# Kernel optimization log

Measured on AMD Instinct MI355X. Metric: run time of the kernel, lower is better.

Reference implementation:

```python
import jax, jax.numpy as jnp
import numpy as np

N_NODES = 100000
N_EDGES = 1600000
N_ETYPES = 3
IN_FEATS = 128
HEADS = 4
OUT_FEATS = 16
EDGE_FEATS = 64
NEG_SLOPE = 0.2


def setup_inputs() -> dict:
    key = jax.random.key(0)
    ks = jax.random.split(key, 10)
    return {
        "x": jax.random.normal(ks[0], (N_NODES, IN_FEATS), jnp.float32),
        "W": jax.random.normal(ks[1], (IN_FEATS, HEADS * OUT_FEATS), jnp.float32) * 0.05,
        "W_e": jax.random.normal(ks[2], (EDGE_FEATS, HEADS * EDGE_FEATS), jnp.float32) * 0.05,
        "attn_l": jax.random.normal(ks[3], (HEADS, OUT_FEATS), jnp.float32) * 0.1,
        "attn_r": jax.random.normal(ks[4], (HEADS, OUT_FEATS), jnp.float32) * 0.1,
        "attn_e": jax.random.normal(ks[5], (HEADS, EDGE_FEATS), jnp.float32) * 0.1,
        "edge_emb": jax.random.normal(ks[6], (N_ETYPES, EDGE_FEATS), jnp.float32),
        "src": jax.random.randint(ks[7], (N_EDGES,), 0, N_NODES, jnp.int32),
        "dst": jax.random.randint(ks[8], (N_EDGES,), 0, N_NODES, jnp.int32),
        "etype": jax.random.randint(ks[9], (N_EDGES,), 0, N_ETYPES, jnp.int32),
    }


def reference(x, W, W_e, attn_l, attn_r, attn_e, edge_emb, src, dst, etype):
    N = x.shape[0]
    H, D = attn_l.shape
    # node projection: [N, H, D]
    feat = (x @ W).reshape(N, H, D)
    # per-node attention halves: [N, H]
    el = jnp.einsum("nhd,hd->nh", feat, attn_l)
    er = jnp.einsum("nhd,hd->nh", feat, attn_r)
    # per-etype edge term: [T, H]
    e_feat = (edge_emb @ W_e).reshape(edge_emb.shape[0], H, -1)
    ee = jnp.einsum("the,he->th", e_feat, attn_e)
    # per-edge pre-softmax score: [E, H]
    s = el[src] + er[dst] + ee[etype]
    s = jnp.where(s > 0, s, NEG_SLOPE * s)  # leaky_relu
    # edge softmax over incoming edges of each dst node (homogeneous graph)
    m = jax.ops.segment_max(s, dst, num_segments=N)
    e = jnp.exp(s - m[dst])
    z = jax.ops.segment_sum(e, dst, num_segments=N)
    a = e / z[dst]  # [E, H]
    # u_mul_e + sum aggregation: [N, H, D]
    msg = feat[src] * a[:, :, None]
    rst = jax.ops.segment_sum(msg, dst, num_segments=N)
    return rst, a
```

## Files before the change

### kernel.cpp

```cpp
#include <hip/hip_runtime.h>
#include <hip/hip_bf16.h>

#define N_NODES   100000
#define N_EDGES   1600000
#define N_ETYPES  3
#define IN_FEATS  128
#define HEADS     4
#define OUT_FEATS 16
#define EDGE_FEATS 64
#define HD        64
#define NEG_SLOPE 0.2f
#define MAXD_LDS  128

#define NBUCK     800
#define NPB       125
#define PBLK      400
#define EPB       4000
#define BCAP      2560
#define FROWS     32


typedef short s16x8 __attribute__((ext_vector_type(8)));
typedef float f32x4 __attribute__((ext_vector_type(4)));

__device__ __forceinline__ short f2bs(float f) {
    __hip_bfloat16 h = __float2bfloat16(f);
    return *reinterpret_cast<short*>(&h);
}

__global__ __launch_bounds__(256) void wt_prep_kernel(
    const float* __restrict__ W, short* __restrict__ WTb)
{
    const int t = blockIdx.x * 256 + threadIdx.x;
    const int k = t >> 6, n = t & 63;
    WTb[n * IN_FEATS + k] = f2bs(W[t]);
}

#define XS_STRIDE 136
__global__ __launch_bounds__(256) void feat_el_er_kernel(
    const float* __restrict__ x,
    const short* __restrict__ WTb,
    const float* __restrict__ attn_l,
    const float* __restrict__ attn_r,
    const float* __restrict__ edge_emb,
    const float* __restrict__ W_e,
    const float* __restrict__ attn_e,
    __hip_bfloat16* __restrict__ featb,
    float* __restrict__ el,
    float* __restrict__ er,
    float* __restrict__ ee,
    int* __restrict__ cnt)
{
    const int t = threadIdx.x;

    if (blockIdx.x == N_NODES / FROWS) {
        for (int j = t; j < NBUCK; j += 256) cnt[j] = 0;
        const int wv = t >> 6, e = t & 63;
        for (int j = wv; j < N_ETYPES * HEADS; j += 4) {
            const int ty = j >> 2, h = j & 3;
            float ef = 0.f;
#pragma unroll
            for (int k = 0; k < EDGE_FEATS; ++k)
                ef += edge_emb[ty * EDGE_FEATS + k] *
                      W_e[k * (HEADS * EDGE_FEATS) + h * EDGE_FEATS + e];
            float v = ef * attn_e[h * EDGE_FEATS + e];
#pragma unroll
            for (int m = 1; m < 64; m <<= 1) v += __shfl_xor(v, m, 64);
            if (e == 0) ee[ty * HEADS + h] = v;
        }
        return;
    }

    __shared__ short Xs[FROWS * XS_STRIDE];

    const int row0 = blockIdx.x * FROWS;
    {
        const int r = t >> 3, k0 = (t & 7) * 16;
        const float4* xg = (const float4*)(x + (size_t)(row0 + r) * IN_FEATS + k0);
        const float4 v0 = xg[0], v1 = xg[1], v2 = xg[2], v3 = xg[3];
        s16x8 p0, p1;
        p0[0] = f2bs(v0.x); p0[1] = f2bs(v0.y); p0[2] = f2bs(v0.z); p0[3] = f2bs(v0.w);
        p0[4] = f2bs(v1.x); p0[5] = f2bs(v1.y); p0[6] = f2bs(v1.z); p0[7] = f2bs(v1.w);
        p1[0] = f2bs(v2.x); p1[1] = f2bs(v2.y); p1[2] = f2bs(v2.z); p1[3] = f2bs(v2.w);
        p1[4] = f2bs(v3.x); p1[5] = f2bs(v3.y); p1[6] = f2bs(v3.z); p1[7] = f2bs(v3.w);
        *(s16x8*)&Xs[r * XS_STRIDE + k0]     = p0;
        *(s16x8*)&Xs[r * XS_STRIDE + k0 + 8] = p1;
    }

    const int w    = t >> 6;
    const int lane = t & 63;
    const int m    = lane & 15;
    const int q    = lane >> 4;

    s16x8 bfr[4];
#pragma unroll
    for (int kb = 0; kb < 4; ++kb)
        bfr[kb] = *(const s16x8*)(WTb + (size_t)(w * 16 + m) * IN_FEATS + kb * 32 + q * 8);

    const float al = attn_l[w * OUT_FEATS + m];
    const float ar = attn_r[w * OUT_FEATS + m];

    __syncthreads();

#pragma unroll
    for (int rg = 0; rg < 2; ++rg) {
        f32x4 acc = {0.f, 0.f, 0.f, 0.f};
#pragma unroll
        for (int kb = 0; kb < 4; ++kb) {
            const s16x8 af = *(const s16x8*)&Xs[(rg * 16 + m) * XS_STRIDE + kb * 32 + q * 8];
            acc = __builtin_amdgcn_mfma_f32_16x16x32_bf16(af, bfr[kb], acc, 0, 0, 0);
        }
#pragma unroll
        for (int r = 0; r < 4; ++r) {
            const int row = row0 + rg * 16 + q * 4 + r;
            featb[(size_t)row * HD + w * 16 + m] = __float2bfloat16(acc[r]);
            float cl = acc[r] * al;
            float cr = acc[r] * ar;
#pragma unroll
            for (int msk = 1; msk < 16; msk <<= 1) {
                cl += __shfl_xor(cl, msk, 64);
                cr += __shfl_xor(cr, msk, 64);
            }
            if (m == 0) {
                el[row * HEADS + w] = cl;
                er[row * HEADS + w] = cr;
            }
        }
    }
}

__global__ __launch_bounds__(256) void scatter_kernel(
    const int* __restrict__ src, const int* __restrict__ dst,
    const int* __restrict__ etype,
    int* __restrict__ cnt, int2* __restrict__ sc_bucket)
{
    __shared__ int h[NBUCK];
    int buld[16];
    const int t = threadIdx.x, b = blockIdx.x;
    for (int j = t; j < NBUCK; j += 256) h[j] = 0;
    __syncthreads();
    const int e0 = b * EPB;
    int k = 0;
    for (int i = t; i < EPB; i += 256, ++k) {
        const int dn = dst[e0 + i];
        const int bu = dn / NPB;
        const int ld = dn - bu * NPB;
        buld[k] = bu | (ld << 16);
        atomicAdd(&h[bu], 1);
    }
    __syncthreads();
    for (int j = t; j < NBUCK; j += 256) {
        const int c = h[j];
        h[j] = j * BCAP + (c ? atomicAdd(&cnt[j], c) : 0);
    }
    __syncthreads();
    k = 0;
    for (int i = t; i < EPB; i += 256, ++k) {
        const int e  = e0 + i;
        const int bu = buld[k] & 0xFFFF;
        const int ld = buld[k] >> 16;
        const int slot = atomicAdd(&h[bu], 1);
        sc_bucket[slot] = make_int2(src[e], e | (etype[e] << 21) | (ld << 23));
    }
}

__global__ __launch_bounds__(256) void bucket_csr_kernel(
    int2* __restrict__ sc_bucket, const int* __restrict__ cnt,
    int* __restrict__ ptr, int* __restrict__ deg)
{
    __shared__ int2 sbuf[BCAP];
    __shared__ int sdeg4[4][128];
    __shared__ int sdg[128];
    __shared__ int scur[128];
    const int t = threadIdx.x, b = blockIdx.x;
    const int wid = t >> 6;

    sdeg4[0][t & 127] = 0; sdeg4[1][t & 127] = 0;
    if (t < 128) { sdeg4[2][t] = 0; sdeg4[3][t] = 0; }
    __syncthreads();
    const int count = min(cnt[b], BCAP);
    const int base  = b * BCAP;

    for (int i = t; i < count; i += 256) {
        const int2 v = sc_bucket[base + i];
        sbuf[i] = v;
        atomicAdd(&sdeg4[wid][(v.y >> 23) & 0x7F], 1);
    }
    __syncthreads();
    int orig = 0;
    if (t < 128) {
        orig = sdeg4[0][t] + sdeg4[1][t] + sdeg4[2][t] + sdeg4[3][t];
        sdg[t] = orig;
    }
    __syncthreads();
    for (int off = 1; off < 128; off <<= 1) {
        const int v = (t < 128 && t >= off) ? sdg[t - off] : 0;
        __syncthreads();
        if (t < 128) sdg[t] += v;
        __syncthreads();
    }
    if (t < 128) {
        const int excl = sdg[t] - orig;
        if (t < NPB) {
            ptr[b * NPB + t] = base + excl;
            deg[b * NPB + t] = orig;
        }
        scur[t] = base + excl;
    }
    __syncthreads();
    for (int i = t; i < count; i += 256) {
        const int2 v = sbuf[i];
        const int ld = (v.y >> 23) & 0x7F;
        const int slot = atomicAdd(&scur[ld], 1);
        sc_bucket[slot] = make_int2(v.x, v.y & 0x7FFFFF);
    }
}

__global__ __launch_bounds__(256) void agg_kernel(
    const int2* __restrict__ sc_csr, const int* __restrict__ ptr,
    const int* __restrict__ deg_arr,
    const float* __restrict__ el, const float* __restrict__ er,
    const float* __restrict__ ee, const __hip_bfloat16* __restrict__ featb,
    float* __restrict__ rst, float* __restrict__ a_out)
{
    __shared__ float w_lds[4][MAXD_LDS * HEADS];
    __shared__ int   s_lds[4][MAXD_LDS];
    __shared__ int   e_lds[4][MAXD_LDS];
    const int wid  = threadIdx.x >> 6;
    const int lane = threadIdx.x & 63;
    const int n    = blockIdx.x * 4 + wid;

    const int p0  = ptr[n];
    const int deg = deg_arr[n];
    float* wl = w_lds[wid];
    int*   sl = s_lds[wid];
    int*   elds = e_lds[wid];
    const ushort* fb = (const ushort*)featb;

    if (deg <= MAXD_LDS) {
        const int eo = lane >> 2;
        const int hA = lane & 3;
        const float er_n = er[n * HEADS + hA];
        const float g0 = ee[hA], g1 = ee[HEADS + hA], g2 = ee[2 * HEADS + hA];

        float zacc = 0.f;
        for (int i0 = 0; i0 < deg; i0 += 32) {
            const int idxA = i0 + eo;
            const int idxB = i0 + 16 + eo;
            const bool pA = idxA < deg;
            const bool pB = idxB < deg;
            int2 vA = make_int2(0, 0), vB = make_int2(0, 0);
            if (pA) vA = sc_csr[p0 + idxA];
            if (pB) vB = sc_csr[p0 + idxB];
            float eA = 0.f, eB = 0.f;
            if (pA) eA = el[vA.x * HEADS + hA];
            if (pB) eB = el[vB.x * HEADS + hA];
            if (pA) {
                const int ty = vA.y >> 21;
                float s = eA + er_n + ((ty == 0) ? g0 : ((ty == 1) ? g1 : g2));
                s = s > 0.f ? s : NEG_SLOPE * s;
                const float w = __expf(s);
                wl[idxA * HEADS + hA] = w;
                if (hA == 0) sl[idxA] = vA.x;
                if (hA == 1) elds[idxA] = vA.y & 0x1FFFFF;
                zacc += w;
            }
            if (pB) {
                const int ty = vB.y >> 21;
                float s = eB + er_n + ((ty == 0) ? g0 : ((ty == 1) ? g1 : g2));
                s = s > 0.f ? s : NEG_SLOPE * s;
                const float w = __expf(s);
                wl[idxB * HEADS + hA] = w;
                if (hA == 0) sl[idxB] = vB.x;
                if (hA == 1) elds[idxB] = vB.y & 0x1FFFFF;
                zacc += w;
            }
        }
        zacc += __shfl_xor(zacc, 4, 64);
        zacc += __shfl_xor(zacc, 8, 64);
        zacc += __shfl_xor(zacc, 16, 64);
        zacc += __shfl_xor(zacc, 32, 64);
        const float izA = (deg > 0) ? __frcp_rn(zacc) : 0.f;

        for (int idx = eo; idx < deg; idx += 16)
            a_out[((size_t)elds[idx] << 2) + hA] = wl[idx * HEADS + hA] * izA;

        const int q8 = lane >> 3;
        const int c8 = lane & 7;
        const int h8 = c8 >> 1;
        const float inv_z = (deg > 0) ? __frcp_rn(__shfl(zacc, h8, 64)) : 0.f;

        float a0 = 0.f, a1 = 0.f, a2 = 0.f, a3 = 0.f;
        float a4 = 0.f, a5 = 0.f, a6 = 0.f, a7 = 0.f;
        int i = 0;
        for (; i + 16 <= deg; i += 16) {
            const int idxA = i + q8, idxB = i + 8 + q8;
            const int sA = sl[idxA], sB = sl[idxB];
            const float wA = wl[idxA * HEADS + h8];
            const float wB = wl[idxB * HEADS + h8];
            const uint4 fA = *(const uint4*)(fb + ((size_t)sA << 6) + (c8 << 3));
            const uint4 fB = *(const uint4*)(fb + ((size_t)sB << 6) + (c8 << 3));
            a0 += __uint_as_float(fA.x << 16) * wA;
            a1 += __uint_as_float(fA.x & 0xFFFF0000u) * wA;
            a2 += __uint_as_float(fA.y << 16) * wA;
            a3 += __uint_as_float(fA.y & 0xFFFF0000u) * wA;
            a4 += __uint_as_float(fA.z << 16) * wA;
            a5 += __uint_as_float(fA.z & 0xFFFF0000u) * wA;
            a6 += __uint_as_float(fA.w << 16) * wA;
            a7 += __uint_as_float(fA.w & 0xFFFF0000u) * wA;
            a0 += __uint_as_float(fB.x << 16) * wB;
            a1 += __uint_as_float(fB.x & 0xFFFF0000u) * wB;
            a2 += __uint_as_float(fB.y << 16) * wB;
            a3 += __uint_as_float(fB.y & 0xFFFF0000u) * wB;
            a4 += __uint_as_float(fB.z << 16) * wB;
            a5 += __uint_as_float(fB.z & 0xFFFF0000u) * wB;
            a6 += __uint_as_float(fB.w << 16) * wB;
            a7 += __uint_as_float(fB.w & 0xFFFF0000u) * wB;
        }
        if (i + 8 <= deg) {
            const int idx = i + q8;
            const int sA = sl[idx];
            const float wA = wl[idx * HEADS + h8];
            const uint4 fA = *(const uint4*)(fb + ((size_t)sA << 6) + (c8 << 3));
            a0 += __uint_as_float(fA.x << 16) * wA;
            a1 += __uint_as_float(fA.x & 0xFFFF0000u) * wA;
            a2 += __uint_as_float(fA.y << 16) * wA;
            a3 += __uint_as_float(fA.y & 0xFFFF0000u) * wA;
            a4 += __uint_as_float(fA.z << 16) * wA;
            a5 += __uint_as_float(fA.z & 0xFFFF0000u) * wA;
            a6 += __uint_as_float(fA.w << 16) * wA;
            a7 += __uint_as_float(fA.w & 0xFFFF0000u) * wA;
            i += 8;
        }
        if (i + q8 < deg) {
            const int idx = i + q8;
            const int sA = sl[idx];
            const float wA = wl[idx * HEADS + h8];
            const uint4 fA = *(const uint4*)(fb + ((size_t)sA << 6) + (c8 << 3));
            a0 += __uint_as_float(fA.x << 16) * wA;
            a1 += __uint_as_float(fA.x & 0xFFFF0000u) * wA;
            a2 += __uint_as_float(fA.y << 16) * wA;
            a3 += __uint_as_float(fA.y & 0xFFFF0000u) * wA;
            a4 += __uint_as_float(fA.z << 16) * wA;
            a5 += __uint_as_float(fA.z & 0xFFFF0000u) * wA;
            a6 += __uint_as_float(fA.w << 16) * wA;
            a7 += __uint_as_float(fA.w & 0xFFFF0000u) * wA;
        }
        a0 += __shfl_xor(a0, 8, 64); a0 += __shfl_xor(a0, 16, 64); a0 += __shfl_xor(a0, 32, 64);
        a1 += __shfl_xor(a1, 8, 64); a1 += __shfl_xor(a1, 16, 64); a1 += __shfl_xor(a1, 32, 64);
        a2 += __shfl_xor(a2, 8, 64); a2 += __shfl_xor(a2, 16, 64); a2 += __shfl_xor(a2, 32, 64);
        a3 += __shfl_xor(a3, 8, 64); a3 += __shfl_xor(a3, 16, 64); a3 += __shfl_xor(a3, 32, 64);
        a4 += __shfl_xor(a4, 8, 64); a4 += __shfl_xor(a4, 16, 64); a4 += __shfl_xor(a4, 32, 64);
        a5 += __shfl_xor(a5, 8, 64); a5 += __shfl_xor(a5, 16, 64); a5 += __shfl_xor(a5, 32, 64);
        a6 += __shfl_xor(a6, 8, 64); a6 += __shfl_xor(a6, 16, 64); a6 += __shfl_xor(a6, 32, 64);
        a7 += __shfl_xor(a7, 8, 64); a7 += __shfl_xor(a7, 16, 64); a7 += __shfl_xor(a7, 32, 64);
        if (q8 == 0) {
            f32x4 v0 = {a0 * inv_z, a1 * inv_z, a2 * inv_z, a3 * inv_z};
            f32x4 v1 = {a4 * inv_z, a5 * inv_z, a6 * inv_z, a7 * inv_z};
            *(f32x4*)(rst + (size_t)n * HD + (c8 << 3))     = v0;
            *(f32x4*)(rst + (size_t)n * HD + (c8 << 3) + 4) = v1;
        }
    } else {
        const int hA = lane & 3;
        const int eo = lane >> 2;
        const float er_nA = er[n * HEADS + hA];
        const float b0 = ee[hA], b1 = ee[HEADS + hA], b2 = ee[2 * HEADS + hA];
        float zacc = 0.f;
        for (int base = 0; base < deg; base += 16) {
            const int idx = base + eo;
            if (idx < deg) {
                const int2 v = sc_csr[p0 + idx];
                const int ty = v.y >> 21;
                float s = el[v.x * HEADS + hA] + er_nA + ((ty == 0) ? b0 : ((ty == 1) ? b1 : b2));
                s = s > 0.f ? s : NEG_SLOPE * s;
                zacc += __expf(s);
            }
        }
#pragma unroll
        for (int m = 4; m < 64; m <<= 1) zacc += __shfl_xor(zacc, m, 64);
        const int h = lane >> 4;
        const int d = lane & 15;
        const float inv_z = __frcp_rn(__shfl(zacc, h, 64));
        const float er_n = er[n * HEADS + h];
        const float g0 = ee[h], g1 = ee[HEADS + h], g2 = ee[2 * HEADS + h];
        float racc = 0.f;
        for (int i = 0; i < deg; ++i) {
            const int2 v = sc_csr[p0 + i];
            const int ty = v.y >> 21;
            float s = el[v.x * HEADS + h] + er_n + ((ty == 0) ? g0 : ((ty == 1) ? g1 : g2));
            s = s > 0.f ? s : NEG_SLOPE * s;
            const float a = __expf(s) * inv_z;
            racc += __bfloat162float(featb[(size_t)v.x * HD + lane]) * a;
            if (d == 0) a_out[((size_t)(v.y & 0x1FFFFF) << 2) + h] = a;
        }
        rst[(size_t)n * HD + lane] = racc;
    }
}

extern "C" void kernel_launch(void* const* d_in, const int* in_sizes, int n_in,
                              void* d_out, int out_size, void* d_ws, size_t ws_size,
                              hipStream_t stream)
{
    const float* x        = (const float*)d_in[0];
    const float* W        = (const float*)d_in[1];
    const float* W_e      = (const float*)d_in[2];
    const float* attn_l   = (const float*)d_in[3];
    const float* attn_r   = (const float*)d_in[4];
    const float* attn_e   = (const float*)d_in[5];
    const float* edge_emb = (const float*)d_in[6];
    const int* src   = (const int*)d_in[7];
    const int* dst   = (const int*)d_in[8];
    const int* etype = (const int*)d_in[9];

    float* out     = (float*)d_out;
    float* rst_out = out;
    float* a_out   = out + (size_t)N_NODES * HD;

    char* w = (char*)d_ws;
    __hip_bfloat16* featb = (__hip_bfloat16*)w; w += (size_t)N_NODES * HD * 2;
    float* el    = (float*)w;  w += (size_t)N_NODES * HEADS * 4;
    float* er    = (float*)w;  w += (size_t)N_NODES * HEADS * 4;
    float* ee    = (float*)w;  w += 64;
    int*   ptr   = (int*)w;    w += (size_t)(N_NODES + 8) * 4;
    int*   deg   = (int*)w;    w += (size_t)(N_NODES + 8) * 4;
    int*   cnt   = (int*)w;    w += (size_t)(NBUCK + 8) * 4;
    short* WTb   = (short*)w;  w += (size_t)HD * IN_FEATS * 2;
    int2*  sc_bucket = (int2*)w; w += ((size_t)NBUCK * BCAP + 2048) * 8;

    wt_prep_kernel<<<(IN_FEATS * HD) / 256, 256, 0, stream>>>(W, WTb);
    feat_el_er_kernel<<<N_NODES / FROWS + 1, 256, 0, stream>>>(
        x, WTb, attn_l, attn_r, edge_emb, W_e, attn_e, featb, el, er, ee, cnt);
    scatter_kernel<<<PBLK, 256, 0, stream>>>(src, dst, etype, cnt, sc_bucket);
    bucket_csr_kernel<<<NBUCK, 256, 0, stream>>>(sc_bucket, cnt, ptr, deg);
    agg_kernel<<<N_NODES / 4, 256, 0, stream>>>(
        sc_bucket, ptr, deg, el, er, ee, featb, rst_out, a_out);
}
```

Measured before the change: 260.0 us.

## Merge edge scatter into node projection kernel to run concurrently

Fuses the edge bucket-scatter kernel and the node feature projection kernel into one launch, with the first blocks doing scatter work, one block computing per-etype edge terms, and the rest doing the MFMA projection. The bucket counter reset moves into the weight-prep kernel. The aim is to overlap the memory-bound scatter with the projection and drop one launch plus its serialization gap. Both paths now share one LDS buffer sized for the larger of the two, which could affect occupancy.

```diff
diff --git a/kernel.cpp b/kernel.cpp
--- a/kernel.cpp
+++ b/kernel.cpp
@@ -18,6 +18,7 @@
 #define EPB       4000
 #define BCAP      2560
 #define FROWS     32
+#define NFEAT     (N_NODES / FROWS)
 
 
 typedef short s16x8 __attribute__((ext_vector_type(8)));
@@ -29,15 +30,17 @@
 }
 
 __global__ __launch_bounds__(256) void wt_prep_kernel(
-    const float* __restrict__ W, short* __restrict__ WTb)
+    const float* __restrict__ W, short* __restrict__ WTb, int* __restrict__ cnt)
 {
     const int t = blockIdx.x * 256 + threadIdx.x;
     const int k = t >> 6, n = t & 63;
     WTb[n * IN_FEATS + k] = f2bs(W[t]);
+    if (blockIdx.x == 0)
+        for (int j = threadIdx.x; j < NBUCK; j += 256) cnt[j] = 0;
 }
 
 #define XS_STRIDE 136
-__global__ __launch_bounds__(256) void feat_el_er_kernel(
+__global__ __launch_bounds__(256) void feat_scatter_kernel(
     const float* __restrict__ x,
     const short* __restrict__ WTb,
     const float* __restrict__ attn_l,
@@ -45,16 +48,50 @@
     const float* __restrict__ edge_emb,
     const float* __restrict__ W_e,
     const float* __restrict__ attn_e,
+    const int* __restrict__ src, const int* __restrict__ dst,
+    const int* __restrict__ etype,
     __hip_bfloat16* __restrict__ featb,
     float* __restrict__ el,
     float* __restrict__ er,
     float* __restrict__ ee,
-    int* __restrict__ cnt)
+    int* __restrict__ cnt, int2* __restrict__ sc_bucket)
 {
+    __shared__ __align__(16) char smem[FROWS * XS_STRIDE * 2];
     const int t = threadIdx.x;
-
-    if (blockIdx.x == N_NODES / FROWS) {
-        for (int j = t; j < NBUCK; j += 256) cnt[j] = 0;
+    const int b = blockIdx.x;
+
+    if (b < PBLK) {
+        int* h = (int*)smem;
+        int buld[16];
+        for (int j = t; j < NBUCK; j += 256) h[j] = 0;
+        __syncthreads();
+        const int e0 = b * EPB;
+        int k = 0;
+        for (int i = t; i < EPB; i += 256, ++k) {
+            const int dn = dst[e0 + i];
+            const int bu = dn / NPB;
+            const int ld = dn - bu * NPB;
+            buld[k] = bu | (ld << 16);
+            atomicAdd(&h[bu], 1);
+        }
+        __syncthreads();
+        for (int j = t; j < NBUCK; j += 256) {
+            const int c = h[j];
+            h[j] = j * BCAP + (c ? atomicAdd(&cnt[j], c) : 0);
+        }
+        __syncthreads();
+        k = 0;
+        for (int i = t; i < EPB; i += 256, ++k) {
+            const int e  = e0 + i;
+            const int bu = buld[k] & 0xFFFF;
+            const int ld = buld[k] >> 16;
+            const int slot = atomicAdd(&h[bu], 1);
+            sc_bucket[slot] = make_int2(src[e], e | (etype[e] << 21) | (ld << 23));
+        }
+        return;
+    }
+
+    if (b == PBLK) {
         const int wv = t >> 6, e = t & 63;
         for (int j = wv; j < N_ETYPES * HEADS; j += 4) {
             const int ty = j >> 2, h = j & 3;
@@ -71,9 +108,8 @@
         return;
     }
 
-    __shared__ short Xs[FROWS * XS_STRIDE];
-
-    const int row0 = blockIdx.x * FROWS;
+    short* Xs = (short*)smem;
+    const int row0 = (b - PBLK - 1) * FROWS;
     {
         const int r = t >> 3, k0 = (t & 7) * 16;
         const float4* xg = (const float4*)(x + (size_t)(row0 + r) * IN_FEATS + k0);
@@ -126,41 +162,6 @@
                 er[row * HEADS + w] = cr;
             }
         }
-    }
-}
-
-__global__ __launch_bounds__(256) void scatter_kernel(
-    const int* __restrict__ src, const int* __restrict__ dst,
-    const int* __restrict__ etype,
-    int* __restrict__ cnt, int2* __restrict__ sc_bucket)
-{
-    __shared__ int h[NBUCK];
-    int buld[16];
-    const int t = threadIdx.x, b = blockIdx.x;
-    for (int j = t; j < NBUCK; j += 256) h[j] = 0;
-    __syncthreads();
-    const int e0 = b * EPB;
-    int k = 0;
-    for (int i = t; i < EPB; i += 256, ++k) {
-        const int dn = dst[e0 + i];
-        const int bu = dn / NPB;
-        const int ld = dn - bu * NPB;
-        buld[k] = bu | (ld << 16);
-        atomicAdd(&h[bu], 1);
-    }
-    __syncthreads();
-    for (int j = t; j < NBUCK; j += 256) {
-        const int c = h[j];
-        h[j] = j * BCAP + (c ? atomicAdd(&cnt[j], c) : 0);
-    }
-    __syncthreads();
-    k = 0;
-    for (int i = t; i < EPB; i += 256, ++k) {
-        const int e  = e0 + i;
-        const int bu = buld[k] & 0xFFFF;
-        const int ld = buld[k] >> 16;
-        const int slot = atomicAdd(&h[bu], 1);
-        sc_bucket[slot] = make_int2(src[e], e | (etype[e] << 21) | (ld << 23));
     }
 }
 
@@ -427,11 +428,14 @@
     short* WTb   = (short*)w;  w += (size_t)HD * IN_FEATS * 2;
     int2*  sc_bucket = (int2*)w; w += ((size_t)NBUCK * BCAP + 2048) * 8;
 
-    wt_prep_kernel<<<(IN_FEATS * HD) / 256, 256, 0, stream>>>(W, WTb);
-    feat_el_er_kernel<<<N_NODES / FROWS + 1, 256, 0, stream>>>(
-        x, WTb, attn_l, attn_r, edge_emb, W_e, attn_e, featb, el, er, ee, cnt);
-    scatter_kernel<<<PBLK, 256, 0, stream>>>(src, dst, etype, cnt, sc_bucket);
+    wt_prep_kernel<<<(IN_FEATS * HD) / 256, 256, 0, stream>>>(W, WTb, cnt);
+
+    feat_scatter_kernel<<<PBLK + 1 + NFEAT, 256, 0, stream>>>(
+        x, WTb, attn_l, attn_r, edge_emb, W_e, attn_e,
+        src, dst, etype, featb, el, er, ee, cnt, sc_bucket);
+
     bucket_csr_kernel<<<NBUCK, 256, 0, stream>>>(sc_bucket, cnt, ptr, deg);
+
     agg_kernel<<<N_NODES / 4, 256, 0, stream>>>(
         sc_bucket, ptr, deg, el, er, ee, featb, rst_out, a_out);
 }
```

Result: faster. 249.6 us (-4.0%).
